# Kernel optimization log

Hardware: AMD Instinct MI355X
Metric: run time of the kernel (lower is better)

Reference implementation:

```python
import jax, jax.numpy as jnp
import numpy as np

N_HEADS = 16
LN_EPS = 1e-6


def _mha(q_in, kv_in, mask, wq, bq, wk, bk, wv, bv, wo, bo):
    B, Sq, D = q_in.shape
    H = N_HEADS
    dh = D // H
    def split(x):  # [B,S,D] -> [B,H,S,dh]
        return x.reshape(B, -1, H, dh).transpose(0, 2, 1, 3)
    q = split(q_in @ wq + bq)
    k = split(kv_in @ wk + bk)
    v = split(kv_in @ wv + bv)
    scores = jnp.einsum('bhqd,bhkd->bhqk', q, k) / jnp.sqrt(jnp.asarray(dh, q.dtype))
    scores = scores + mask * (-1e9)
    attn = jax.nn.softmax(scores, axis=-1)
    out = jnp.einsum('bhqk,bhkd->bhqd', attn, v)
    out = out.transpose(0, 2, 1, 3).reshape(B, Sq, D)
    return out @ wo + bo


def _layer_norm(x, gamma, beta):
    mu = jnp.mean(x, axis=-1, keepdims=True)
    var = jnp.mean(jnp.square(x - mu), axis=-1, keepdims=True)
    return (x - mu) * jax.lax.rsqrt(var + LN_EPS) * gamma + beta


def setup_inputs() -> dict:
    key = jax.random.key(0)
    B, S_dec, S_enc, D, F = 4, 1024, 1024, 1024, 4096
    ks = jax.random.split(key, 16)
    s = 0.02
    inp = {
        'inputs': jax.random.normal(ks[0], (B, S_dec, D), jnp.float32),
        'enc_outputs': jax.random.normal(ks[1], (B, S_enc, D), jnp.float32),
        # causal look-ahead mask: 1 above diagonal -> -1e9 added to scores
        'mask_1': jnp.triu(jnp.ones((S_dec, S_dec), jnp.float32), k=1)[None, None],
        'mask_2': jnp.zeros((B, 1, 1, S_enc), jnp.float32),
    }
    names = ['wq1', 'wk1', 'wv1', 'wo1', 'wq2', 'wk2', 'wv2', 'wo2']
    for i, n in enumerate(names):
        inp[n] = jax.random.normal(ks[2 + i], (D, D), jnp.float32) * s
        inp['b' + n[1:]] = jnp.zeros((D,), jnp.float32)
    inp['w_ff1'] = jax.random.normal(ks[10], (D, F), jnp.float32) * s
    inp['b_ff1'] = jnp.zeros((F,), jnp.float32)
    inp['w_ff2'] = jax.random.normal(ks[11], (F, D), jnp.float32) * s
    inp['b_ff2'] = jnp.zeros((D,), jnp.float32)
    for i in (1, 2, 3):
        inp[f'g{i}'] = jnp.ones((D,), jnp.float32)
        inp[f'beta{i}'] = jnp.zeros((D,), jnp.float32)
    return inp


def reference(inputs, enc_outputs, mask_1, mask_2,
              wq1, bq1, wk1, bk1, wv1, bv1, wo1, bo1,
              wq2, bq2, wk2, bk2, wv2, bv2, wo2, bo2,
              w_ff1, b_ff1, w_ff2, b_ff2,
              g1, beta1, g2, beta2, g3, beta3):
    # causal self-attention + residual + LN (dropout inactive at inference)
    attn = _mha(inputs, inputs, mask_1, wq1, bq1, wk1, bk1, wv1, bv1, wo1, bo1)
    attn = _layer_norm(attn + inputs, g1, beta1)
    # encoder-decoder cross-attention + residual + LN
    attn2 = _mha(attn, enc_outputs, mask_2, wq2, bq2, wk2, bk2, wv2, bv2, wo2, bo2)
    attn2 = _layer_norm(attn2 + attn, g2, beta2)
    # FFN + residual + LN
    h = jax.nn.relu(attn2 @ w_ff1 + b_ff1)
    h = h @ w_ff2 + b_ff2
    return _layer_norm(h + attn2, g3, beta3)
```

## Files before the change

kernel.cpp:

```cpp
#include <hip/hip_runtime.h>
#include <stdint.h>

typedef unsigned short ushort_t;
typedef __attribute__((ext_vector_type(8))) short bf16x8;
typedef __attribute__((ext_vector_type(4))) float f32x4;
typedef __attribute__((ext_vector_type(4))) unsigned short us4;

#define DEV __device__ __forceinline__

DEV unsigned short f2bf(float f) {
  union { float f; unsigned u; } x; x.f = f;
  unsigned r = x.u + 0x7fffu + ((x.u >> 16) & 1u);
  return (unsigned short)(r >> 16);
}

DEV void gload16(const void* g, void* l) {
  __builtin_amdgcn_global_load_lds(
      (const __attribute__((address_space(1))) unsigned int*)g,
      (__attribute__((address_space(3))) unsigned int*)l, 16, 0, 0);
}

#define MFMA16 __builtin_amdgcn_mfma_f32_16x16x32_bf16

__global__ __launch_bounds__(256) void cast_bf16_kernel(
    const float* __restrict__ x, ushort_t* __restrict__ y, int n4) {
  int i = blockIdx.x * 256 + threadIdx.x;
  if (i >= n4) return;
  float4 v = ((const float4*)x)[i];
  us4 o; o.x = f2bf(v.x); o.y = f2bf(v.y); o.z = f2bf(v.z); o.w = f2bf(v.w);
  ((us4*)y)[i] = o;
}

__global__ __launch_bounds__(256) void reduce_cast_kernel(
    const float* __restrict__ p0, const float* __restrict__ p1,
    ushort_t* __restrict__ y, int n4) {
  int i = blockIdx.x * 256 + threadIdx.x;
  if (i >= n4) return;
  float4 a = ((const float4*)p0)[i];
  float4 b = ((const float4*)p1)[i];
  us4 o; o.x = f2bf(a.x + b.x); o.y = f2bf(a.y + b.y);
  o.z = f2bf(a.z + b.z); o.w = f2bf(a.w + b.w);
  ((us4*)y)[i] = o;
}

__global__ __launch_bounds__(256) void transpose_cast_kernel(
    const float* __restrict__ W, ushort_t* __restrict__ dst, int K, int N) {
  __shared__ float tile[64][65];
  int n0 = blockIdx.x * 64, k0 = blockIdx.y * 64;
  int tid = threadIdx.x;
#pragma unroll
  for (int it = 0; it < 16; ++it) {
    int idx = it * 256 + tid; int r = idx >> 6, c = idx & 63;
    tile[r][c] = W[(size_t)(k0 + r) * N + n0 + c];
  }
  __syncthreads();
#pragma unroll
  for (int it = 0; it < 16; ++it) {
    int idx = it * 256 + tid; int r = idx >> 6, c = idx & 63;
    dst[(size_t)(n0 + r) * K + k0 + c] = f2bf(tile[c][r]);
  }
}

struct Src8 { const float* p[8]; };
__global__ __launch_bounds__(256) void transpose_cast8_kernel(
    Src8 s, ushort_t* __restrict__ dst) {
  __shared__ float tile[64][65];
  const float* W = s.p[blockIdx.z];
  ushort_t* out = dst + (size_t)blockIdx.z * 1048576;
  int n0 = blockIdx.x * 64, k0 = blockIdx.y * 64;
  int tid = threadIdx.x;
#pragma unroll
  for (int it = 0; it < 16; ++it) {
    int idx = it * 256 + tid; int r = idx >> 6, c = idx & 63;
    tile[r][c] = W[(size_t)(k0 + r) * 1024 + n0 + c];
  }
  __syncthreads();
#pragma unroll
  for (int it = 0; it < 16; ++it) {
    int idx = it * 256 + tid; int r = idx >> 6, c = idx & 63;
    out[(size_t)(n0 + r) * 1024 + k0 + c] = f2bf(tile[c][r]);
  }
}

__global__ __launch_bounds__(256) void transpose_v_kernel(
    const ushort_t* __restrict__ V, int ldv, ushort_t* __restrict__ vT) {
  __shared__ ushort_t tile[64][65];
  int s0 = blockIdx.x * 64;
  int bh = blockIdx.y;
  int b = bh >> 4, h = bh & 15;
  int tid = threadIdx.x;
#pragma unroll
  for (int it = 0; it < 4; ++it) {
    int idx = it * 256 + tid; int r = idx >> 4, c = (idx & 15) * 4;
    us4 v = *(const us4*)&V[(size_t)(b * 1024 + s0 + r) * ldv + h * 64 + c];
    tile[r][c] = v.x; tile[r][c + 1] = v.y; tile[r][c + 2] = v.z; tile[r][c + 3] = v.w;
  }
  __syncthreads();
#pragma unroll
  for (int it = 0; it < 4; ++it) {
    int idx = it * 256 + tid; int r = idx >> 4, c = (idx & 15) * 4;
    us4 o; o.x = tile[c][r]; o.y = tile[c + 1][r]; o.z = tile[c + 2][r]; o.w = tile[c + 3][r];
    *(us4*)&vT[((size_t)bh * 64 + r) * 1024 + s0 + c] = o;
  }
}

template <int WF32, int WB16, int RELU>
__global__ __launch_bounds__(256, 2) void gemm_bt(
    const ushort_t* __restrict__ A, const ushort_t* __restrict__ Bt,
    const float* __restrict__ b0, const float* __restrict__ b1,
    const float* __restrict__ b2, const float* __restrict__ b3,
    float* __restrict__ Cf, ushort_t* __restrict__ Cb,
    int M, int N, int K, int Ks, long long pstr) {
  __shared__ ushort_t sA[4096];
  __shared__ ushort_t sB[4096];
  const int tid = threadIdx.x;
  const int w = tid >> 6, lane = tid & 63;
  const int lrow = lane & 15, lk = lane >> 4;
  const int m0 = blockIdx.x * 128, n0 = blockIdx.y * 128;
  const int kz = blockIdx.z * Ks;
  const int wr = w >> 1, wc = w & 1;
  f32x4 acc[4][4] = {};
  const int brow0 = (w * 1024 + lane * 16) >> 6;
  const int kbyte = (lane * 16) & 63;

  for (int kt = kz; kt < kz + Ks; kt += 32) {
    __syncthreads();
    const ushort_t* ga = A + (size_t)(m0 + brow0) * K + kt + (kbyte >> 1);
    gload16(ga, (char*)sA + w * 1024);
    gload16(ga + (size_t)64 * K, (char*)sA + 4096 + w * 1024);
    const ushort_t* gb = Bt + (size_t)(n0 + brow0) * K + kt + (kbyte >> 1);
    gload16(gb, (char*)sB + w * 1024);
    gload16(gb + (size_t)64 * K, (char*)sB + 4096 + w * 1024);
    __syncthreads();
    bf16x8 aF[4], bF[4];
#pragma unroll
    for (int t = 0; t < 4; ++t) {
      aF[t] = *(const bf16x8*)((const char*)sA + ((wr * 64 + t * 16 + lrow) << 6) + (lk << 4));
      bF[t] = *(const bf16x8*)((const char*)sB + ((wc * 64 + t * 16 + lrow) << 6) + (lk << 4));
    }
#pragma unroll
    for (int mt = 0; mt < 4; ++mt)
#pragma unroll
      for (int nt = 0; nt < 4; ++nt)
        acc[mt][nt] = MFMA16(aF[mt], bF[nt], acc[mt][nt], 0, 0, 0);
  }
  float* Cfz = Cf + (long long)blockIdx.z * pstr;
#pragma unroll
  for (int nt = 0; nt < 4; ++nt) {
    int col = n0 + wc * 64 + nt * 16 + lrow;
    int seg = col >> 10;
    const float* bp = seg == 0 ? b0 : seg == 1 ? b1 : seg == 2 ? b2 : b3;
    float bv = bp[col & 1023];
    if (blockIdx.z != 0) bv = 0.f;
#pragma unroll
    for (int mt = 0; mt < 4; ++mt) {
      int rowb = m0 + wr * 64 + mt * 16 + lk * 4;
#pragma unroll
      for (int j = 0; j < 4; ++j) {
        float v = acc[mt][nt][j] + bv;
        if (RELU) v = fmaxf(v, 0.f);
        size_t idx = (size_t)(rowb + j) * N + col;
        if (WF32) Cfz[idx] = v;
        if (WB16) Cb[idx] = f2bf(v);
      }
    }
  }
}

template <int WF32, int WB16, int RELU>
__global__ __launch_bounds__(512, 2) void gemm256(
    const ushort_t* __restrict__ A, const ushort_t* __restrict__ Bt,
    const float* __restrict__ b0, const float* __restrict__ b1,
    const float* __restrict__ b2, const float* __restrict__ b3,
    float* __restrict__ Cf, ushort_t* __restrict__ Cb,
    int M, int N, int K, int Ks, long long pstr) {
  extern __shared__ char L[];
  const int tid = threadIdx.x;
  const int w = tid >> 6, lane = tid & 63;
  const int lrow = lane & 15, lk = lane >> 4;
  const int wm = w >> 2, wn = w & 3;
  const int m0 = blockIdx.x * 256, n0 = blockIdx.y * 256;
  const int kz = blockIdx.z * Ks;
  const int nt = Ks >> 6;

  const int rL = lane >> 2;
  const int csw = (lane & 3) ^ (rL & 3);
  const ushort_t* srcA = A + (size_t)(m0 + w * 16 + rL) * K + kz + csw * 8;
  const ushort_t* srcB = Bt + (size_t)(n0 + w * 16 + rL) * K + kz + csw * 8;
  const int dstw = w * 1024;

#define STG(M_, KK_, T_)                                                      \
  do {                                                                        \
    const ushort_t* g0 = ((M_) ? srcB : srcA) + (size_t)(T_) * 64 + (KK_) * 32; \
    char* d_ = L + (((T_) & 1) << 16) + ((M_) << 15) + ((KK_) << 14) + dstw;  \
    gload16(g0, d_);                                                          \
    gload16(g0 + (size_t)128 * K, d_ + 8192);                                 \
  } while (0)

  f32x4 acc[8][4] = {};
  const int lkx16 = (lk ^ (lrow & 3)) << 4;
  const int arow = (wm * 128 + lrow) << 6;
  const int brow = (wn * 64 + lrow) << 6;

  STG(0, 0, 0); STG(1, 0, 0); STG(0, 1, 0); STG(1, 1, 0);
  STG(0, 0, 1); STG(1, 0, 1); STG(0, 1, 1);
  asm volatile("s_waitcnt vmcnt(6)" ::: "memory");
  __builtin_amdgcn_s_barrier();

  for (int t = 0; t < nt; ++t) {
    const int buf = (t & 1) << 16;
    bf16x8 aF[8], bF0, bF1;
    {
      const char* pA = L + buf + arow + lkx16;
#pragma unroll
      for (int m = 0; m < 8; ++m) aF[m] = *(const bf16x8*)(pA + m * 1024);
      const char* pB = L + buf + 32768 + brow + lkx16;
      bF0 = *(const bf16x8*)pB;
      bF1 = *(const bf16x8*)(pB + 1024);
      if (t + 1 < nt) STG(1, 1, t + 1);
      __builtin_amdgcn_s_barrier();
      __builtin_amdgcn_s_setprio(1);
#pragma unroll
      for (int m = 0; m < 8; ++m) {
        acc[m][0] = MFMA16(aF[m], bF0, acc[m][0], 0, 0, 0);
        acc[m][1] = MFMA16(aF[m], bF1, acc[m][1], 0, 0, 0);
      }
      __builtin_amdgcn_s_setprio(0);
      __builtin_amdgcn_s_barrier();
    }
    {
      const char* pB = L + buf + 32768 + brow + lkx16;
      bF0 = *(const bf16x8*)(pB + 2048);
      bF1 = *(const bf16x8*)(pB + 3072);
      if (t + 2 < nt) STG(0, 0, t + 2);
      __builtin_amdgcn_s_barrier();
      __builtin_amdgcn_s_setprio(1);
#pragma unroll
      for (int m = 0; m < 8; ++m) {
        acc[m][2] = MFMA16(aF[m], bF0, acc[m][2], 0, 0, 0);
        acc[m][3] = MFMA16(aF[m], bF1, acc[m][3], 0, 0, 0);
      }
      __builtin_amdgcn_s_setprio(0);
      __builtin_amdgcn_s_barrier();
    }
    {
      const char* pA = L + buf + 16384 + arow + lkx16;
#pragma unroll
      for (int m = 0; m < 8; ++m) aF[m] = *(const bf16x8*)(pA + m * 1024);
      const char* pB = L + buf + 32768 + 16384 + brow + lkx16;
      bF0 = *(const bf16x8*)pB;
      bF1 = *(const bf16x8*)(pB + 1024);
      if (t + 2 < nt) STG(1, 0, t + 2);
      __builtin_amdgcn_s_barrier();
      __builtin_amdgcn_s_setprio(1);
#pragma unroll
      for (int m = 0; m < 8; ++m) {
        acc[m][0] = MFMA16(aF[m], bF0, acc[m][0], 0, 0, 0);
        acc[m][1] = MFMA16(aF[m], bF1, acc[m][1], 0, 0, 0);
      }
      __builtin_amdgcn_s_setprio(0);
      __builtin_amdgcn_s_barrier();
    }
    {
      const char* pB = L + buf + 32768 + 16384 + brow + lkx16;
      bF0 = *(const bf16x8*)(pB + 2048);
      bF1 = *(const bf16x8*)(pB + 3072);
      if (t + 2 < nt) {
        STG(0, 1, t + 2);
        asm volatile("s_waitcnt vmcnt(6)" ::: "memory");
      } else {
        asm volatile("s_waitcnt vmcnt(0)" ::: "memory");
      }
      __builtin_amdgcn_s_barrier();
      __builtin_amdgcn_s_setprio(1);
#pragma unroll
      for (int m = 0; m < 8; ++m) {
        acc[m][2] = MFMA16(aF[m], bF0, acc[m][2], 0, 0, 0);
        acc[m][3] = MFMA16(aF[m], bF1, acc[m][3], 0, 0, 0);
      }
      __builtin_amdgcn_s_setprio(0);
      __builtin_amdgcn_s_barrier();
    }
  }
#undef STG

  float* Cfz = Cf + (long long)blockIdx.z * pstr;
#pragma unroll
  for (int n = 0; n < 4; ++n) {
    int col = n0 + wn * 64 + n * 16 + lrow;
    int seg = col >> 10;
    const float* bp = seg == 0 ? b0 : seg == 1 ? b1 : seg == 2 ? b2 : b3;
    float bv = bp[col & 1023];
    if (blockIdx.z != 0) bv = 0.f;
#pragma unroll
    for (int m = 0; m < 8; ++m) {
      int rowb = m0 + wm * 128 + m * 16 + lk * 4;
#pragma unroll
      for (int j = 0; j < 4; ++j) {
        float v = acc[m][n][j] + bv;
        if (RELU) v = fmaxf(v, 0.f);
        size_t idx = (size_t)(rowb + j) * N + col;
        if (WF32) Cfz[idx] = v;
        if (WB16) Cb[idx] = f2bf(v);
      }
    }
  }
}

template <int CAUSAL>
__global__ __launch_bounds__(256, 4) void attn_kernel(
    const ushort_t* __restrict__ Q, int ldq,
    const ushort_t* __restrict__ Kp, int ldk,
    const ushort_t* __restrict__ vT,
    const float* __restrict__ mask2,
    ushort_t* __restrict__ O) {
  __shared__ ushort_t sK[2][4096];
  __shared__ ushort_t sV[2][4096];
  __shared__ ushort_t sP[4][1024];
  const int x = blockIdx.x;
  const int qb = ((x & 1) << 3) | ((x & 2) << 1) | ((x & 4) >> 1) | ((x & 8) >> 3);
  const int bh = blockIdx.y;
  const int b = bh >> 4, h = bh & 15;
  const int tid = threadIdx.x, w = tid >> 6, lane = tid & 63;
  const int lrow = lane & 15, lk = lane >> 4;

  const ushort_t* qptr = Q + (size_t)(b * 1024 + qb * 64 + w * 16 + lrow) * ldq + h * 64 + lk * 8;
  bf16x8 qF0 = *(const bf16x8*)qptr;
  bf16x8 qF1 = *(const bf16x8*)(qptr + 32);
  f32x4 oacc[4] = {};
  float m_ = -3.0e38f, l_ = 0.f;
  const int nkb = CAUSAL ? (qb + 1) : 16;
  const float C = 0.18033688011112042f;

  const int sr = w * 16 + (lane >> 3);
  const int scb = (((lane & 7) ^ (lane >> 3)) * 16);
  const ushort_t* kbase = Kp + (size_t)(b * 1024 + sr) * ldk + h * 64 + (scb >> 1);
  const ushort_t* vbase = vT + ((size_t)bh * 64 + sr) * 1024 + (scb >> 1);
  char* dstK0 = (char*)sK[0] + w * 2048;
  char* dstV0 = (char*)sV[0] + w * 2048;

#define STAGE(kb_, bufi)                                              \
  do {                                                                \
    const ushort_t* gk = kbase + (size_t)(kb_) * 64 * ldk;            \
    gload16(gk, dstK0 + (bufi) * 8192);                               \
    gload16(gk + (size_t)8 * ldk, dstK0 + (bufi) * 8192 + 1024);      \
    const ushort_t* gv = vbase + (kb_) * 64;                          \
    gload16(gv, dstV0 + (bufi) * 8192);                               \
    gload16(gv + (size_t)8 * 1024, dstV0 + (bufi) * 8192 + 1024);     \
  } while (0)

  STAGE(0, 0);
  const int swz = (lrow & 7) << 4;

  for (int kb = 0; kb < nkb; ++kb) {
    const int buf = kb & 1;
    __syncthreads();
    if (kb + 1 < nkb) STAGE(kb + 1, buf ^ 1);

    const char* kB = (const char*)sK[buf];
    const char* vB = (const char*)sV[buf];
    f32x4 sc[4];
    __builtin_amdgcn_s_setprio(1);
#pragma unroll
    for (int kt = 0; kt < 4; ++kt) {
      const char* rp = kB + ((kt * 16 + lrow) << 7);
      bf16x8 k0 = *(const bf16x8*)(rp + ((lk * 16) ^ swz));
      bf16x8 k1 = *(const bf16x8*)(rp + ((64 + lk * 16) ^ swz));
      f32x4 z = {};
      z = MFMA16(k0, qF0, z, 0, 0, 0);
      sc[kt] = MFMA16(k1, qF1, z, 0, 0, 0);
    }
    __builtin_amdgcn_s_setprio(0);
    if (CAUSAL) {
      if (kb == qb) {
        int ql = w * 16 + lrow;
#pragma unroll
        for (int kt = 0; kt < 4; ++kt)
#pragma unroll
          for (int j = 0; j < 4; ++j)
            if (kt * 16 + lk * 4 + j > ql) sc[kt][j] = -3.0e38f;
      }
    } else {
#pragma unroll
      for (int kt = 0; kt < 4; ++kt) {
        float4 mv = *(const float4*)&mask2[b * 1024 + kb * 64 + kt * 16 + lk * 4];
        sc[kt][0] = fmaf(mv.x, -8e9f, sc[kt][0]);
        sc[kt][1] = fmaf(mv.y, -8e9f, sc[kt][1]);
        sc[kt][2] = fmaf(mv.z, -8e9f, sc[kt][2]);
        sc[kt][3] = fmaf(mv.w, -8e9f, sc[kt][3]);
      }
    }
    float pmax = fmaxf(fmaxf(fmaxf(sc[0][0], sc[0][1]), fmaxf(sc[0][2], sc[0][3])),
                       fmaxf(fmaxf(sc[1][0], sc[1][1]), fmaxf(sc[1][2], sc[1][3])));
    pmax = fmaxf(pmax, fmaxf(fmaxf(fmaxf(sc[2][0], sc[2][1]), fmaxf(sc[2][2], sc[2][3])),
                             fmaxf(fmaxf(sc[3][0], sc[3][1]), fmaxf(sc[3][2], sc[3][3]))));
    pmax = fmaxf(pmax, __shfl_xor(pmax, 16));
    pmax = fmaxf(pmax, __shfl_xor(pmax, 32));
    if (__any(pmax - m_ > 64.f)) {
      float mnew = fmaxf(m_, pmax);
      float scale = __builtin_exp2f((m_ - mnew) * C);
      l_ *= scale;
      m_ = mnew;
#pragma unroll
      for (int j = 0; j < 4; ++j) {
        float sj = __shfl(scale, lk * 4 + j);
        oacc[0][j] *= sj; oacc[1][j] *= sj; oacc[2][j] *= sj; oacc[3][j] *= sj;
      }
    }
    const float mC = m_ * C;
    float ps = 0.f;
#pragma unroll
    for (int kt = 0; kt < 4; ++kt)
#pragma unroll
      for (int j = 0; j < 4; ++j) {
        float e = __builtin_exp2f(fmaf(sc[kt][j], C, -mC));
        sc[kt][j] = e;
        ps += e;
      }
    ps += __shfl_xor(ps, 16);
    ps += __shfl_xor(ps, 32);
    l_ += ps;
    char* bp = (char*)sP[w] + lrow * 128;
#pragma unroll
    for (int kt = 0; kt < 4; ++kt) {
      unsigned d0, d1;
      asm("v_cvt_pk_bf16_f32 %0, %1, %2" : "=v"(d0) : "v"(sc[kt][0]), "v"(sc[kt][1]));
      asm("v_cvt_pk_bf16_f32 %0, %1, %2" : "=v"(d1) : "v"(sc[kt][2]), "v"(sc[kt][3]));
      uint2 dd; dd.x = d0; dd.y = d1;
      *(uint2*)(bp + ((kt * 32 + lk * 8) ^ swz)) = dd;
    }
    bf16x8 pF0 = *(const bf16x8*)(bp + ((lk * 16) ^ swz));
    bf16x8 pF1 = *(const bf16x8*)(bp + ((64 + lk * 16) ^ swz));
    __builtin_amdgcn_s_setprio(1);
#pragma unroll
    for (int t = 0; t < 4; ++t) {
      const char* rp = vB + ((t * 16 + lrow) << 7);
      bf16x8 v0 = *(const bf16x8*)(rp + ((lk * 16) ^ swz));
      bf16x8 v1 = *(const bf16x8*)(rp + ((64 + lk * 16) ^ swz));
      oacc[t] = MFMA16(pF0, v0, oacc[t], 0, 0, 0);
      oacc[t] = MFMA16(pF1, v1, oacc[t], 0, 0, 0);
    }
    __builtin_amdgcn_s_setprio(0);
  }
#undef STAGE
#pragma unroll
  for (int j = 0; j < 4; ++j) {
    float lj = __shfl(l_, lk * 4 + j);
    float invl = 1.f / lj;
    int row = qb * 64 + w * 16 + lk * 4 + j;
    ushort_t* op = O + (size_t)(b * 1024 + row) * 1024 + h * 64;
#pragma unroll
    for (int t = 0; t < 4; ++t) op[t * 16 + lrow] = f2bf(oacc[t][j] * invl);
  }
}

template <int WB16, int NPART>
__global__ __launch_bounds__(256) void ln_kernel(
    const float* __restrict__ p0, const float* __restrict__ p1,
    const float* __restrict__ p2, const float* __restrict__ p3,
    const float* __restrict__ r,
    const float* __restrict__ g, const float* __restrict__ be,
    float* __restrict__ yf, ushort_t* __restrict__ yb) {
  int row = blockIdx.x, tid = threadIdx.x;
  size_t off = (size_t)row * 1024;
  float4 va = ((const float4*)(p0 + off))[tid];
  if (NPART >= 2) {
    float4 t = ((const float4*)(p1 + off))[tid];
    va.x += t.x; va.y += t.y; va.z += t.z; va.w += t.w;
  }
  if (NPART >= 4) {
    float4 t2 = ((const float4*)(p2 + off))[tid];
    float4 t3 = ((const float4*)(p3 + off))[tid];
    va.x += t2.x + t3.x; va.y += t2.y + t3.y;
    va.z += t2.z + t3.z; va.w += t2.w + t3.w;
  }
  float4 vb = ((const float4*)(r + off))[tid];
  float x0 = va.x + vb.x, x1 = va.y + vb.y, x2 = va.z + vb.z, x3 = va.w + vb.w;
  float s = x0 + x1 + x2 + x3;
  float s2 = x0 * x0 + x1 * x1 + x2 * x2 + x3 * x3;
#pragma unroll
  for (int o = 1; o < 64; o <<= 1) { s += __shfl_xor(s, o); s2 += __shfl_xor(s2, o); }
  __shared__ float sh[8];
  if ((tid & 63) == 0) { sh[tid >> 6] = s; sh[4 + (tid >> 6)] = s2; }
  __syncthreads();
  s = sh[0] + sh[1] + sh[2] + sh[3];
  s2 = sh[4] + sh[5] + sh[6] + sh[7];
  float mu = s * 0.0009765625f;
  float var = s2 * 0.0009765625f - mu * mu;
  float inv = rsqrtf(var + 1e-6f);
  float4 gv = ((const float4*)g)[tid];
  float4 bv = ((const float4*)be)[tid];
  float y0 = (x0 - mu) * inv * gv.x + bv.x;
  float y1 = (x1 - mu) * inv * gv.y + bv.y;
  float y2 = (x2 - mu) * inv * gv.z + bv.z;
  float y3 = (x3 - mu) * inv * gv.w + bv.w;
  ((float4*)(yf + off))[tid] = make_float4(y0, y1, y2, y3);
  if (WB16) {
    us4 o; o.x = f2bf(y0); o.y = f2bf(y1); o.z = f2bf(y2); o.w = f2bf(y3);
    ((us4*)(yb + off))[tid] = o;
  }
}

extern "C" void kernel_launch(void* const* d_in, const int* in_sizes, int n_in,
                              void* d_out, int out_size, void* d_ws, size_t ws_size,
                              hipStream_t stream) {
  (void)in_sizes; (void)n_in; (void)out_size; (void)ws_size;
  const float* inputs = (const float*)d_in[0];
  const float* enc    = (const float*)d_in[1];
  const float* mask2  = (const float*)d_in[3];
  const float* wq1 = (const float*)d_in[4];  const float* bq1 = (const float*)d_in[5];
  const float* wk1 = (const float*)d_in[6];  const float* bk1 = (const float*)d_in[7];
  const float* wv1 = (const float*)d_in[8];  const float* bv1 = (const float*)d_in[9];
  const float* wo1 = (const float*)d_in[10]; const float* bo1 = (const float*)d_in[11];
  const float* wq2 = (const float*)d_in[12]; const float* bq2 = (const float*)d_in[13];
  const float* wk2 = (const float*)d_in[14]; const float* bk2 = (const float*)d_in[15];
  const float* wv2 = (const float*)d_in[16]; const float* bv2 = (const float*)d_in[17];
  const float* wo2 = (const float*)d_in[18]; const float* bo2 = (const float*)d_in[19];
  const float* wff1 = (const float*)d_in[20]; const float* bff1 = (const float*)d_in[21];
  const float* wff2 = (const float*)d_in[22]; const float* bff2 = (const float*)d_in[23];
  const float* g1 = (const float*)d_in[24]; const float* be1 = (const float*)d_in[25];
  const float* g2 = (const float*)d_in[26]; const float* be2 = (const float*)d_in[27];
  const float* g3 = (const float*)d_in[28]; const float* be3 = (const float*)d_in[29];

  char* ws = (char*)d_ws;
  const size_t MB = 1024 * 1024;
  const size_t W1M = 1048576;
  ushort_t* wt    = (ushort_t*)ws;
  ushort_t* xb    = (ushort_t*)(ws + 32 * MB);
  ushort_t* encb  = (ushort_t*)(ws + 40 * MB);
  ushort_t* qkvb  = (ushort_t*)(ws + 48 * MB);
  ushort_t* vtb   = (ushort_t*)(ws + 72 * MB);
  ushort_t* attnb = (ushort_t*)(ws + 80 * MB);
  ushort_t* y1b   = (ushort_t*)(ws + 88 * MB);
  ushort_t* y2b   = (ushort_t*)(ws + 96 * MB);
  float*    c1f   = (float*)(ws + 104 * MB);
  float*    p48f  = (float*)(ws + 48 * MB);
  float*    y1f   = (float*)(ws + 120 * MB);
  float*    y2f   = (float*)(ws + 136 * MB);
  ushort_t* q2b   = (ushort_t*)(ws + 32 * MB);
  ushort_t* kv2b  = (ushort_t*)(ws + 56 * MB);
  ushort_t* hb    = (ushort_t*)(ws + 32 * MB);
  float*    pff   = (float*)(ws + 72 * MB);
  float* outf = (float*)d_out;
  const long long PELEMS = 4 * 1024 * 1024;
  const long long P48OFF = (long long)(p48f - c1f);

  cast_bf16_kernel<<<4096, 256, 0, stream>>>(inputs, xb, 1048576);
  cast_bf16_kernel<<<4096, 256, 0, stream>>>(enc, encb, 1048576);
  Src8 s8; s8.p[0] = wq1; s8.p[1] = wk1; s8.p[2] = wv1; s8.p[3] = wo1;
           s8.p[4] = wq2; s8.p[5] = wk2; s8.p[6] = wv2; s8.p[7] = wo2;
  transpose_cast8_kernel<<<dim3(16, 16, 8), 256, 0, stream>>>(s8, wt);
  transpose_cast_kernel<<<dim3(64, 16), 256, 0, stream>>>(wff1, wt + 8 * W1M, 1024, 4096);
  transpose_cast_kernel<<<dim3(16, 64), 256, 0, stream>>>(wff2, wt + 12 * W1M, 4096, 1024);

  gemm256<0, 1, 0><<<dim3(16, 12, 1), 512, 131072, stream>>>(
      xb, wt, bq1, bk1, bv1, bv1, nullptr, qkvb, 4096, 3072, 1024, 1024, 0);
  transpose_v_kernel<<<dim3(16, 64), 256, 0, stream>>>(qkvb + 2048, 3072, vtb);
  attn_kernel<1><<<dim3(16, 64), 256, 0, stream>>>(
      qkvb, 3072, qkvb + 1024, 3072, vtb, nullptr, attnb);
  gemm_bt<1, 0, 0><<<dim3(32, 8, 2), 256, 0, stream>>>(
      attnb, wt + 3 * W1M, bo1, bo1, bo1, bo1, c1f, nullptr, 4096, 1024, 1024, 512, P48OFF);
  ln_kernel<1, 2><<<4096, 256, 0, stream>>>(c1f, p48f, nullptr, nullptr,
                                            inputs, g1, be1, y1f, y1b);

  gemm_bt<1, 0, 0><<<dim3(32, 8, 2), 256, 0, stream>>>(
      y1b, wt + 4 * W1M, bq2, bq2, bq2, bq2, c1f, nullptr, 4096, 1024, 1024, 512, P48OFF);
  reduce_cast_kernel<<<4096, 256, 0, stream>>>(c1f, p48f, q2b, 1048576);
  gemm_bt<0, 1, 0><<<dim3(32, 16, 1), 256, 0, stream>>>(
      encb, wt + 5 * W1M, bk2, bv2, bk2, bk2, nullptr, kv2b, 4096, 2048, 1024, 1024, 0);
  transpose_v_kernel<<<dim3(16, 64), 256, 0, stream>>>(kv2b + 1024, 2048, vtb);
  attn_kernel<0><<<dim3(16, 64), 256, 0, stream>>>(
      q2b, 1024, kv2b, 2048, vtb, mask2, attnb);
  gemm_bt<1, 0, 0><<<dim3(32, 8, 2), 256, 0, stream>>>(
      attnb, wt + 7 * W1M, bo2, bo2, bo2, bo2, c1f, nullptr, 4096, 1024, 1024, 512, P48OFF);
  ln_kernel<1, 2><<<4096, 256, 0, stream>>>(c1f, p48f, nullptr, nullptr,
                                            y1f, g2, be2, y2f, y2b);

  gemm256<0, 1, 1><<<dim3(16, 16, 1), 512, 131072, stream>>>(
      y2b, wt + 8 * W1M, bff1, bff1 + 1024, bff1 + 2048, bff1 + 3072,
      nullptr, hb, 4096, 4096, 1024, 1024, 0);
  gemm256<1, 0, 0><<<dim3(16, 4, 4), 512, 131072, stream>>>(
      hb, wt + 12 * W1M, bff2, bff2, bff2, bff2, pff, nullptr,
      4096, 1024, 4096, 1024, PELEMS);
  ln_kernel<0, 4><<<4096, 256, 0, stream>>>(pff, pff + PELEMS, pff + 2 * PELEMS,
                                            pff + 3 * PELEMS, y2f, g3, be3, outf, nullptr);
}
```

Baseline: 389.8 us.

## Restage gemm256 LDS tiles as full-k rows with XOR swizzle, reorder attention grid

The gemm256 shared-memory layout changes from two 32-wide k halves per operand to a single 64-wide k row (128 bytes) with an 8-way XOR swizzle. Each stage issues four 16-byte async loads per operand instead of several half-tile stages, which simplifies the prefetch schedule and wait counts. Launch bounds drop from 2 to 1 block per CU, giving the compiler more registers but lowering occupancy. The attention grid is transposed so blockIdx.x indexes batch-head and blockIdx.y the query block, and the causal bit-reversed query-block order is removed, which may hurt load balance.

```diff
diff --git a/kernel.cpp b/kernel.cpp
--- a/kernel.cpp
+++ b/kernel.cpp
@@ -168,7 +168,7 @@
 }
 
 template <int WF32, int WB16, int RELU>
-__global__ __launch_bounds__(512, 2) void gemm256(
+__global__ __launch_bounds__(512, 1) void gemm256(
     const ushort_t* __restrict__ A, const ushort_t* __restrict__ Bt,
     const float* __restrict__ b0, const float* __restrict__ b1,
     const float* __restrict__ b2, const float* __restrict__ b3,
@@ -183,41 +183,43 @@
   const int kz = blockIdx.z * Ks;
   const int nt = Ks >> 6;
 
-  const int rL = lane >> 2;
-  const int csw = (lane & 3) ^ (rL & 3);
-  const ushort_t* srcA = A + (size_t)(m0 + w * 16 + rL) * K + kz + csw * 8;
-  const ushort_t* srcB = Bt + (size_t)(n0 + w * 16 + rL) * K + kz + csw * 8;
+  const int srow = w * 8 + (lane >> 3);
+  const int gsw = (lane & 7) ^ ((lane >> 3) & 7);
+  const ushort_t* srcA = A + (size_t)(m0 + srow) * K + kz + gsw * 8;
+  const ushort_t* srcB = Bt + (size_t)(n0 + srow) * K + kz + gsw * 8;
   const int dstw = w * 1024;
 
-#define STG(M_, KK_, T_)                                                      \
-  do {                                                                        \
-    const ushort_t* g0 = ((M_) ? srcB : srcA) + (size_t)(T_) * 64 + (KK_) * 32; \
-    char* d_ = L + (((T_) & 1) << 16) + ((M_) << 15) + ((KK_) << 14) + dstw;  \
-    gload16(g0, d_);                                                          \
-    gload16(g0 + (size_t)128 * K, d_ + 8192);                                 \
+#define STG(M_, T_)                                                   \
+  do {                                                                \
+    const ushort_t* g0 = ((M_) ? srcB : srcA) + (size_t)(T_) * 64;    \
+    char* d_ = L + (((T_) & 1) << 16) + ((M_) << 15) + dstw;          \
+    gload16(g0, d_);                                                  \
+    gload16(g0 + (size_t)64 * K, d_ + 8192);                          \
+    gload16(g0 + (size_t)128 * K, d_ + 16384);                        \
+    gload16(g0 + (size_t)192 * K, d_ + 24576);                        \
   } while (0)
 
   f32x4 acc[8][4] = {};
-  const int lkx16 = (lk ^ (lrow & 3)) << 4;
-  const int arow = (wm * 128 + lrow) << 6;
-  const int brow = (wn * 64 + lrow) << 6;
-
-  STG(0, 0, 0); STG(1, 0, 0); STG(0, 1, 0); STG(1, 1, 0);
-  STG(0, 0, 1); STG(1, 0, 1); STG(0, 1, 1);
-  asm volatile("s_waitcnt vmcnt(6)" ::: "memory");
+  const int swz = (lrow & 7) << 4;
+  const int k0b = (lk << 4) ^ swz;
+  const int k1b = (64 + (lk << 4)) ^ swz;
+  const int aBase = (wm * 128 + lrow) << 7;
+  const int bBase = ((wn * 64 + lrow) << 7) + 32768;
+
+  STG(0, 0); STG(1, 0); STG(0, 1);
+  asm volatile("s_waitcnt vmcnt(4)" ::: "memory");
   __builtin_amdgcn_s_barrier();
 
   for (int t = 0; t < nt; ++t) {
     const int buf = (t & 1) << 16;
+    const char* base = L + buf;
     bf16x8 aF[8], bF0, bF1;
     {
-      const char* pA = L + buf + arow + lkx16;
-#pragma unroll
-      for (int m = 0; m < 8; ++m) aF[m] = *(const bf16x8*)(pA + m * 1024);
-      const char* pB = L + buf + 32768 + brow + lkx16;
-      bF0 = *(const bf16x8*)pB;
-      bF1 = *(const bf16x8*)(pB + 1024);
-      if (t + 1 < nt) STG(1, 1, t + 1);
+#pragma unroll
+      for (int m = 0; m < 8; ++m) aF[m] = *(const bf16x8*)(base + aBase + m * 2048 + k0b);
+      bF0 = *(const bf16x8*)(base + bBase + k0b);
+      bF1 = *(const bf16x8*)(base + bBase + 2048 + k0b);
+      if (t + 1 < nt) STG(1, t + 1);
       __builtin_amdgcn_s_barrier();
       __builtin_amdgcn_s_setprio(1);
 #pragma unroll
@@ -229,10 +231,8 @@
       __builtin_amdgcn_s_barrier();
     }
     {
-      const char* pB = L + buf + 32768 + brow + lkx16;
-      bF0 = *(const bf16x8*)(pB + 2048);
-      bF1 = *(const bf16x8*)(pB + 3072);
-      if (t + 2 < nt) STG(0, 0, t + 2);
+      bF0 = *(const bf16x8*)(base + bBase + 4096 + k0b);
+      bF1 = *(const bf16x8*)(base + bBase + 6144 + k0b);
       __builtin_amdgcn_s_barrier();
       __builtin_amdgcn_s_setprio(1);
 #pragma unroll
@@ -244,13 +244,10 @@
       __builtin_amdgcn_s_barrier();
     }
     {
-      const char* pA = L + buf + 16384 + arow + lkx16;
-#pragma unroll
-      for (int m = 0; m < 8; ++m) aF[m] = *(const bf16x8*)(pA + m * 1024);
-      const char* pB = L + buf + 32768 + 16384 + brow + lkx16;
-      bF0 = *(const bf16x8*)pB;
-      bF1 = *(const bf16x8*)(pB + 1024);
-      if (t + 2 < nt) STG(1, 0, t + 2);
+#pragma unroll
+      for (int m = 0; m < 8; ++m) aF[m] = *(const bf16x8*)(base + aBase + m * 2048 + k1b);
+      bF0 = *(const bf16x8*)(base + bBase + k1b);
+      bF1 = *(const bf16x8*)(base + bBase + 2048 + k1b);
       __builtin_amdgcn_s_barrier();
       __builtin_amdgcn_s_setprio(1);
 #pragma unroll
@@ -262,12 +259,11 @@
       __builtin_amdgcn_s_barrier();
     }
     {
-      const char* pB = L + buf + 32768 + 16384 + brow + lkx16;
-      bF0 = *(const bf16x8*)(pB + 2048);
-      bF1 = *(const bf16x8*)(pB + 3072);
+      bF0 = *(const bf16x8*)(base + bBase + 4096 + k1b);
+      bF1 = *(const bf16x8*)(base + bBase + 6144 + k1b);
       if (t + 2 < nt) {
-        STG(0, 1, t + 2);
-        asm volatile("s_waitcnt vmcnt(6)" ::: "memory");
+        STG(0, t + 2);
+        asm volatile("s_waitcnt vmcnt(4)" ::: "memory");
       } else {
         asm volatile("s_waitcnt vmcnt(0)" ::: "memory");
       }
@@ -317,9 +313,7 @@
   __shared__ ushort_t sK[2][4096];
   __shared__ ushort_t sV[2][4096];
   __shared__ ushort_t sP[4][1024];
-  const int x = blockIdx.x;
-  const int qb = ((x & 1) << 3) | ((x & 2) << 1) | ((x & 4) >> 1) | ((x & 8) >> 3);
-  const int bh = blockIdx.y;
+  const int bh = blockIdx.x, qb = blockIdx.y;
   const int b = bh >> 4, h = bh & 15;
   const int tid = threadIdx.x, w = tid >> 6, lane = tid & 63;
   const int lrow = lane & 15, lk = lane >> 4;
@@ -556,7 +550,7 @@
   gemm256<0, 1, 0><<<dim3(16, 12, 1), 512, 131072, stream>>>(
       xb, wt, bq1, bk1, bv1, bv1, nullptr, qkvb, 4096, 3072, 1024, 1024, 0);
   transpose_v_kernel<<<dim3(16, 64), 256, 0, stream>>>(qkvb + 2048, 3072, vtb);
-  attn_kernel<1><<<dim3(16, 64), 256, 0, stream>>>(
+  attn_kernel<1><<<dim3(64, 16), 256, 0, stream>>>(
       qkvb, 3072, qkvb + 1024, 3072, vtb, nullptr, attnb);
   gemm_bt<1, 0, 0><<<dim3(32, 8, 2), 256, 0, stream>>>(
       attnb, wt + 3 * W1M, bo1, bo1, bo1, bo1, c1f, nullptr, 4096, 1024, 1024, 512, P48OFF);
@@ -569,7 +563,7 @@
   gemm_bt<0, 1, 0><<<dim3(32, 16, 1), 256, 0, stream>>>(
       encb, wt + 5 * W1M, bk2, bv2, bk2, bk2, nullptr, kv2b, 4096, 2048, 1024, 1024, 0);
   transpose_v_kernel<<<dim3(16, 64), 256, 0, stream>>>(kv2b + 1024, 2048, vtb);
-  attn_kernel<0><<<dim3(16, 64), 256, 0, stream>>>(
+  attn_kernel<0><<<dim3(64, 16), 256, 0, stream>>>(
       q2b, 1024, kv2b, 2048, vtb, mask2, attnb);
   gemm_bt<1, 0, 0><<<dim3(32, 8, 2), 256, 0, stream>>>(
       attnb, wt + 7 * W1M, bo2, bo2, bo2, bo2, c1f, nullptr, 4096, 1024, 1024, 512, P48OFF);
```

After: 363.6 us. 1.07x faster.
